# Kernel tuning notes

Hardware: AMD Instinct MI355X
Metric: run time of the kernel (lower is better)

Reference implementation:

```python
import jax, jax.numpy as jnp
import numpy as np

N = 50000      # input_dim == output_dim
E = 800000     # nnz in sparse weight (original: 12300 from w_ind.mat)
B = 64         # batch


def setup_inputs() -> dict:
    key = jax.random.key(0)
    k1, k2, k3, k4, k5 = jax.random.split(key, 5)
    inputs = jax.random.normal(k1, (B, N), dtype=jnp.float32)
    # truncated-normal(std=0.01) approximated by scaled normal
    W3 = 0.01 * jax.random.normal(k2, (E,), dtype=jnp.float32)
    b = jnp.zeros((N,), dtype=jnp.float32)
    # velocity = 1250 * row of CSV -> positive scale vector
    velocity = 1250.0 * jax.random.uniform(k3, (N,), dtype=jnp.float32)
    I = jax.random.randint(k4, (E,), 0, N, dtype=jnp.int64)  # row (dest) index
    J = jax.random.randint(k5, (E,), 0, N, dtype=jnp.int64)  # col (source) index
    return {"inputs": inputs, "W3": W3, "b": b, "velocity": velocity, "I": I, "J": J}


def reference(inputs, W3, b, velocity, I, J):
    # sparse W[i,j] = W3[e] scaled by velocity broadcast along rows -> * velocity[J]
    wv = W3 * velocity[J]                       # [E]
    # out = (W_sparse @ inputs^T)^T + b  == scatter-add over rows I
    contrib = inputs[:, J] * wv[None, :]        # [B, E] gather + scale
    out = jnp.zeros((inputs.shape[0], velocity.shape[0]), inputs.dtype)
    out = out.at[:, I].add(contrib)             # [B, N] scatter-add
    return out + b
```

## Files before the change

### kernel.cpp

```cpp
#include <hip/hip_runtime.h>


#define BATCH 64
#define QROWS 64
#define PCHUNK 8192
#define GCH 512
#define CAP 512

typedef unsigned long long ull;

__global__ void k_prep(const float* __restrict__ in, float* __restrict__ in_T,
                       int* __restrict__ coarse_hist, int NC, int N) {
    const int gid = blockIdx.x * 256 + threadIdx.x;
    if (gid < NC) coarse_hist[gid] = 0;

    __shared__ float tile[64 * 65];
    const int n0 = blockIdx.x * 64;
    const int t  = threadIdx.x;
    const int x  = t & 63;
    const int r  = t >> 6;
    for (int b = r; b < BATCH; b += 4) {
        float v = 0.f;
        if (n0 + x < N) v = in[(size_t)b * N + n0 + x];
        tile[x * 65 + b] = v;
    }
    __syncthreads();
    for (int xr = r; xr < 64; xr += 4) {
        if (n0 + xr < N) in_T[(size_t)(n0 + xr) * BATCH + x] = tile[xr * 65 + x];
    }
}

__global__ void __launch_bounds__(1024) k_hist(const int* __restrict__ I,
                                               int* __restrict__ coarse_hist,
                                               int E, int NC) {
    __shared__ int h[1024];
    const int t = threadIdx.x;
    for (int c = t; c < NC; c += 1024) h[c] = 0;
    __syncthreads();
    const int e0 = blockIdx.x * PCHUNK;
    int e1 = e0 + PCHUNK; if (e1 > E) e1 = E;
    for (int e = e0 + t; e < e1; e += 1024) atomicAdd(&h[I[e] >> 6], 1);
    __syncthreads();
    for (int c = t; c < NC; c += 1024) if (h[c]) atomicAdd(&coarse_hist[c], h[c]);
}

__global__ void __launch_bounds__(1024) k_scan(const int* __restrict__ coarse_hist,
                                               int* __restrict__ coarse_base,
                                               int* __restrict__ gcursor, int NC) {
    __shared__ int sh[1024];
    const int t = threadIdx.x;
    const int v = (t < NC) ? coarse_hist[t] : 0;
    sh[t] = v;
    __syncthreads();
    for (int off = 1; off < 1024; off <<= 1) {
        const int u = (t >= off) ? sh[t - off] : 0;
        __syncthreads();
        sh[t] += u;
        __syncthreads();
    }
    if (t < NC) { coarse_base[t] = sh[t] - v; gcursor[t] = sh[t] - v; }
    if (t == NC - 1) coarse_base[NC] = sh[t];
}

__global__ void __launch_bounds__(1024) k_partition(
        const int* __restrict__ I, const int* __restrict__ J,
        const float* __restrict__ W3, const float* __restrict__ velocity,
        int* __restrict__ gcursor, ull* __restrict__ part, int E, int NC) {
    __shared__ int hist[1024];
    __shared__ int base[1024];
    const int t = threadIdx.x;
    for (int c = t; c < NC; c += 1024) hist[c] = 0;
    __syncthreads();
    const int e0 = blockIdx.x * PCHUNK;
    int e1 = e0 + PCHUNK; if (e1 > E) e1 = E;

    for (int e = e0 + t; e < e1; e += 1024) atomicAdd(&hist[I[e] >> 6], 1);
    __syncthreads();
    for (int c = t; c < NC; c += 1024) {
        const int cnt = hist[c];
        base[c] = cnt ? atomicAdd(&gcursor[c], cnt) : 0;
        hist[c] = 0;
    }
    __syncthreads();
    for (int e = e0 + t; e < e1; e += 1024) {
        const int   i = I[e];
        const int   j = J[e];
        const float w = W3[e] * velocity[j];
        const int   c = i >> 6;
        const int   r = atomicAdd(&hist[c], 1);
        part[(size_t)base[c] + r] = ((ull)__float_as_uint(w) << 32)
                                  | ((ull)((unsigned)(i & 63) << 16) | (unsigned)j);
    }
}

__global__ void __launch_bounds__(512) k_gather(
        const float* __restrict__ in_T, const ull* __restrict__ part,
        const int* __restrict__ coarse_base, const float* __restrict__ bias,
        float* __restrict__ out, int N) {
    __shared__ float tile[64 * 65];
    __shared__ ull   bins[8][CAP];
    __shared__ int   cnt[8];
    const int t    = threadIdx.x;
    const int lane = t & 63;
    const int w    = t >> 6;
    const int c    = blockIdx.x;

    for (int idx = t; idx < 64 * 65; idx += 512) tile[idx] = 0.f;

    const int beg = coarse_base[c];
    const int end = coarse_base[c + 1];

    for (int cb = beg; cb < end; cb += GCH) {
        if (t < 8) cnt[t] = 0;
        __syncthreads();

        const int e = cb + t;
        if (e < end) {
            const ull rec = part[e];
            const int bin = (int)(((unsigned)rec >> 19) & 7u);
            const int r = atomicAdd(&cnt[bin], 1);
            bins[bin][r] = rec;
        }
        __syncthreads();

        const int cw = cnt[w];
        for (int base = 0; base < cw; base += 64) {
            int cc = cw - base; if (cc > 64) cc = 64;
            ull rec = 0ull;
            if (lane < cc) rec = bins[w][base + lane];
            const int rlo = (int)(unsigned)(rec & 0xffffffffu);
            const int rhi = (int)(unsigned)(rec >> 32);
            for (int k0 = 0; k0 < cc; k0 += 8) {
                float v[8], wv[8]; int li[8];
                #pragma unroll
                for (int u = 0; u < 8; ++u) {
                    const int k = k0 + u;
                    const unsigned ij = (unsigned)__shfl(rlo, k);
                    wv[u] = __uint_as_float((unsigned)__shfl(rhi, k));
                    li[u] = (int)((ij >> 16) & 7u);
                    const int j = (int)(ij & 0xffffu);
                    v[u] = in_T[j * BATCH + lane];
                }
                #pragma unroll
                for (int u = 0; u < 8; ++u) {
                    tile[(w * 8 + li[u]) * 65 + lane] += v[u] * wv[u];
                }
            }
        }
        __syncthreads();
    }
    __syncthreads();

    const int n0  = c * QROWS;
    const int row = t & 63;
    const int bq  = t >> 6;
    const int n = n0 + row;
    if (n < N) {
        const float bv = bias[n];
        for (int b = bq; b < BATCH; b += 8)
            out[(size_t)b * N + n] = tile[row * 65 + b] + bv;
    }
}

__global__ void k_edge_scatter_direct(const float* __restrict__ in,
                                      const float* __restrict__ W3,
                                      const float* __restrict__ velocity,
                                      const int* __restrict__ I,
                                      const int* __restrict__ J,
                                      float* __restrict__ out, int N, int E) {
    const int lane = threadIdx.x & 63;
    const long wave   = (long)blockIdx.x * (blockDim.x >> 6) + (threadIdx.x >> 6);
    const long nwaves = (long)gridDim.x * (blockDim.x >> 6);
    for (long base = wave * 64; base < E; base += nwaves * 64) {
        const long e = base + lane;
        int iv = 0, jv = 0; float wvv = 0.f;
        if (e < E) { iv = I[e]; jv = J[e]; wvv = W3[e] * velocity[jv]; }
        const int cnt = (int)((E - base) < 64 ? (E - base) : 64);
        for (int k = 0; k < cnt; ++k) {
            const int   ii = __shfl(iv, k);
            const int   jj = __shfl(jv, k);
            const float wvx = __shfl(wvv, k);
            const float val = in[(size_t)lane * N + jj] * wvx;
            atomicAdd(&out[(size_t)lane * N + ii], val);
        }
    }
}

__global__ void k_add_bias(const float* __restrict__ bias, float* __restrict__ out, int N, int total) {
    int idx = blockIdx.x * blockDim.x + threadIdx.x;
    if (idx < total) out[idx] += bias[idx % N];
}

extern "C" void kernel_launch(void* const* d_in, const int* in_sizes, int n_in,
                              void* d_out, int out_size, void* d_ws, size_t ws_size,
                              hipStream_t stream) {
    const float* inputs   = (const float*)d_in[0];
    const float* W3       = (const float*)d_in[1];
    const float* bias     = (const float*)d_in[2];
    const float* velocity = (const float*)d_in[3];
    const int*   I        = (const int*)d_in[4];
    const int*   J        = (const int*)d_in[5];
    const int E = in_sizes[1];
    const int N = in_sizes[3];
    float* out = (float*)d_out;

    const size_t mat_elems = (size_t)N * BATCH;
    const int NC   = (N + QROWS - 1) / QROWS;
    const int nb_n = (N + 63) / 64;
    const int nb_e = (E + PCHUNK - 1) / PCHUNK;

    const size_t need = mat_elems * sizeof(float)
                      + (size_t)E * sizeof(ull)
                      + (size_t)(NC + (NC + 1) + NC) * sizeof(int);

    if (ws_size >= need && N <= 65535 && NC <= 1024) {
        float* in_T        = (float*)d_ws;
        ull*   part        = (ull*)(in_T + mat_elems);
        int*   coarse_hist = (int*)(part + E);
        int*   coarse_base = coarse_hist + NC;
        int*   gcursor     = coarse_base + NC + 1;

        k_prep     <<<nb_n, 256,  0, stream>>>(inputs, in_T, coarse_hist, NC, N);
        k_hist     <<<nb_e, 1024, 0, stream>>>(I, coarse_hist, E, NC);
        k_scan     <<<1,    1024, 0, stream>>>(coarse_hist, coarse_base, gcursor, NC);
        k_partition<<<nb_e, 1024, 0, stream>>>(I, J, W3, velocity, gcursor, part, E, NC);
        k_gather   <<<NC,   512,  0, stream>>>(in_T, part, coarse_base, bias, out, N);
    } else {
        hipMemsetAsync(out, 0, (size_t)out_size * sizeof(float), stream);
        const int waves_needed   = (E + 63) / 64;
        const int scatter_blocks = (waves_needed + 3) / 4;
        k_edge_scatter_direct<<<scatter_blocks, 256, 0, stream>>>(inputs, W3, velocity, I, J, out, N, E);
        k_add_bias<<<(out_size + 255) / 256, 256, 0, stream>>>(bias, out, N, out_size);
    }
}
```

Before: 161.8 us.

## Bin gather edges per output row and accumulate in registers; single-pass partition

The gather kernel now bins each chunk's edges by their exact destination row (64 bins, capped at 32 entries each, with an overflow list). Each wave accumulates its 8 rows in registers instead of doing read-modify-write on a shared-memory tile. The partition kernel now reads each edge once into registers, ranking it while counting, rather than making two passes over the chunk. Chunk and block sizes shrink to 2048 edges and 512 threads, which gives more blocks. The overflow path is scanned serially by every wave, which could be costly for skewed rows.

Result: faster. 148.9 us (-8.0%).

```diff
diff --git a/kernel.cpp b/kernel.cpp
--- a/kernel.cpp
+++ b/kernel.cpp
@@ -3,9 +3,10 @@
 
 #define BATCH 64
 #define QROWS 64
-#define PCHUNK 8192
+#define PCHUNK 2048
 #define GCH 512
-#define CAP 512
+#define BCAP 32
+#define BSTR 33
 
 typedef unsigned long long ull;
 
@@ -30,18 +31,18 @@
     }
 }
 
-__global__ void __launch_bounds__(1024) k_hist(const int* __restrict__ I,
-                                               int* __restrict__ coarse_hist,
-                                               int E, int NC) {
+__global__ void __launch_bounds__(512) k_hist(const int* __restrict__ I,
+                                              int* __restrict__ coarse_hist,
+                                              int E, int NC) {
     __shared__ int h[1024];
     const int t = threadIdx.x;
-    for (int c = t; c < NC; c += 1024) h[c] = 0;
+    for (int c = t; c < NC; c += 512) h[c] = 0;
     __syncthreads();
     const int e0 = blockIdx.x * PCHUNK;
     int e1 = e0 + PCHUNK; if (e1 > E) e1 = E;
-    for (int e = e0 + t; e < e1; e += 1024) atomicAdd(&h[I[e] >> 6], 1);
-    __syncthreads();
-    for (int c = t; c < NC; c += 1024) if (h[c]) atomicAdd(&coarse_hist[c], h[c]);
+    for (int e = e0 + t; e < e1; e += 512) atomicAdd(&h[I[e] >> 6], 1);
+    __syncthreads();
+    for (int c = t; c < NC; c += 512) if (h[c]) atomicAdd(&coarse_hist[c], h[c]);
 }
 
 __global__ void __launch_bounds__(1024) k_scan(const int* __restrict__ coarse_hist,
@@ -62,93 +63,134 @@
     if (t == NC - 1) coarse_base[NC] = sh[t];
 }
 
-__global__ void __launch_bounds__(1024) k_partition(
+__global__ void __launch_bounds__(512) k_partition(
         const int* __restrict__ I, const int* __restrict__ J,
         const float* __restrict__ W3, const float* __restrict__ velocity,
         int* __restrict__ gcursor, ull* __restrict__ part, int E, int NC) {
     __shared__ int hist[1024];
     __shared__ int base[1024];
     const int t = threadIdx.x;
-    for (int c = t; c < NC; c += 1024) hist[c] = 0;
+    for (int c = t; c < NC; c += 512) hist[c] = 0;
     __syncthreads();
     const int e0 = blockIdx.x * PCHUNK;
     int e1 = e0 + PCHUNK; if (e1 > E) e1 = E;
 
-    for (int e = e0 + t; e < e1; e += 1024) atomicAdd(&hist[I[e] >> 6], 1);
-    __syncthreads();
-    for (int c = t; c < NC; c += 1024) {
+    ull  rec[4];
+    int  cb[4];
+    int  rk[4];
+    bool ok[4];
+    #pragma unroll
+    for (int u = 0; u < 4; ++u) {
+        const int e = e0 + u * 512 + t;
+        ok[u] = (e < e1);
+        cb[u] = 0; rk[u] = 0; rec[u] = 0ull;
+        if (ok[u]) {
+            const int   i = I[e];
+            const int   j = J[e];
+            const float w = W3[e] * velocity[j];
+            cb[u] = i >> 6;
+            rk[u] = atomicAdd(&hist[cb[u]], 1);
+            rec[u] = ((ull)__float_as_uint(w) << 32)
+                   | ((ull)((unsigned)(i & 63) << 16) | (unsigned)j);
+        }
+    }
+    __syncthreads();
+    for (int c = t; c < NC; c += 512) {
         const int cnt = hist[c];
         base[c] = cnt ? atomicAdd(&gcursor[c], cnt) : 0;
-        hist[c] = 0;
-    }
-    __syncthreads();
-    for (int e = e0 + t; e < e1; e += 1024) {
-        const int   i = I[e];
-        const int   j = J[e];
-        const float w = W3[e] * velocity[j];
-        const int   c = i >> 6;
-        const int   r = atomicAdd(&hist[c], 1);
-        part[(size_t)base[c] + r] = ((ull)__float_as_uint(w) << 32)
-                                  | ((ull)((unsigned)(i & 63) << 16) | (unsigned)j);
-    }
+    }
+    __syncthreads();
+    #pragma unroll
+    for (int u = 0; u < 4; ++u)
+        if (ok[u]) part[(size_t)base[cb[u]] + rk[u]] = rec[u];
 }
 
 __global__ void __launch_bounds__(512) k_gather(
         const float* __restrict__ in_T, const ull* __restrict__ part,
         const int* __restrict__ coarse_base, const float* __restrict__ bias,
         float* __restrict__ out, int N) {
-    __shared__ float tile[64 * 65];
-    __shared__ ull   bins[8][CAP];
-    __shared__ int   cnt[8];
+    __shared__ ull smem[64 * BSTR + GCH];
+    __shared__ int cnt[64];
+    __shared__ int ocnt;
+    ull* const bins = smem;
+    ull* const ovf  = smem + 64 * BSTR;
+    float* const tile = (float*)smem;
+
     const int t    = threadIdx.x;
     const int lane = t & 63;
     const int w    = t >> 6;
     const int c    = blockIdx.x;
 
-    for (int idx = t; idx < 64 * 65; idx += 512) tile[idx] = 0.f;
-
     const int beg = coarse_base[c];
     const int end = coarse_base[c + 1];
 
+    float acc[8];
+    #pragma unroll
+    for (int r = 0; r < 8; ++r) acc[r] = 0.f;
+
     for (int cb = beg; cb < end; cb += GCH) {
-        if (t < 8) cnt[t] = 0;
+        __syncthreads();
+        if (t < 64) cnt[t] = 0;
+        if (t == 0) ocnt = 0;
         __syncthreads();
 
         const int e = cb + t;
         if (e < end) {
             const ull rec = part[e];
-            const int bin = (int)(((unsigned)rec >> 19) & 7u);
-            const int r = atomicAdd(&cnt[bin], 1);
-            bins[bin][r] = rec;
-        }
-        __syncthreads();
-
-        const int cw = cnt[w];
-        for (int base = 0; base < cw; base += 64) {
-            int cc = cw - base; if (cc > 64) cc = 64;
-            ull rec = 0ull;
-            if (lane < cc) rec = bins[w][base + lane];
-            const int rlo = (int)(unsigned)(rec & 0xffffffffu);
-            const int rhi = (int)(unsigned)(rec >> 32);
-            for (int k0 = 0; k0 < cc; k0 += 8) {
-                float v[8], wv[8]; int li[8];
-                #pragma unroll
-                for (int u = 0; u < 8; ++u) {
-                    const int k = k0 + u;
-                    const unsigned ij = (unsigned)__shfl(rlo, k);
-                    wv[u] = __uint_as_float((unsigned)__shfl(rhi, k));
-                    li[u] = (int)((ij >> 16) & 7u);
-                    const int j = (int)(ij & 0xffffu);
-                    v[u] = in_T[j * BATCH + lane];
+            const int li = (int)(((unsigned)rec >> 16) & 63u);
+            const int r = atomicAdd(&cnt[li], 1);
+            if (r < BCAP) bins[li * BSTR + r] = rec;
+            else          ovf[atomicAdd(&ocnt, 1)] = rec;
+        }
+        __syncthreads();
+
+        #pragma unroll
+        for (int r8 = 0; r8 < 8; ++r8) {
+            const int row = w * 8 + r8;
+            int n = cnt[row]; if (n > BCAP) n = BCAP;
+            const ull* bp = &bins[row * BSTR];
+            float a = acc[r8];
+            int k = 0;
+            for (; k + 4 <= n; k += 4) {
+                const ull r0 = bp[k], r1 = bp[k + 1], r2 = bp[k + 2], r3 = bp[k + 3];
+                const float v0 = in_T[(int)((unsigned)r0 & 0xffffu) * BATCH + lane];
+                const float v1 = in_T[(int)((unsigned)r1 & 0xffffu) * BATCH + lane];
+                const float v2 = in_T[(int)((unsigned)r2 & 0xffffu) * BATCH + lane];
+                const float v3 = in_T[(int)((unsigned)r3 & 0xffffu) * BATCH + lane];
+                a += v0 * __uint_as_float((unsigned)(r0 >> 32));
+                a += v1 * __uint_as_float((unsigned)(r1 >> 32));
+                a += v2 * __uint_as_float((unsigned)(r2 >> 32));
+                a += v3 * __uint_as_float((unsigned)(r3 >> 32));
+            }
+            for (; k < n; ++k) {
+                const ull rr = bp[k];
+                a += in_T[(int)((unsigned)rr & 0xffffu) * BATCH + lane]
+                   * __uint_as_float((unsigned)(rr >> 32));
+            }
+            acc[r8] = a;
+        }
+
+        const int oc = ocnt;
+        if (oc > 0) {
+            #pragma unroll
+            for (int r8 = 0; r8 < 8; ++r8) {
+                const int row = w * 8 + r8;
+                float a = acc[r8];
+                for (int k = 0; k < oc; ++k) {
+                    const ull rr = ovf[k];
+                    if ((int)(((unsigned)rr >> 16) & 63u) == row)
+                        a += in_T[(int)((unsigned)rr & 0xffffu) * BATCH + lane]
+                           * __uint_as_float((unsigned)(rr >> 32));
                 }
-                #pragma unroll
-                for (int u = 0; u < 8; ++u) {
-                    tile[(w * 8 + li[u]) * 65 + lane] += v[u] * wv[u];
-                }
+                acc[r8] = a;
             }
         }
-        __syncthreads();
-    }
+    }
+
+    __syncthreads();
+    #pragma unroll
+    for (int r8 = 0; r8 < 8; ++r8)
+        tile[(w * 8 + r8) * 65 + lane] = acc[r8];
     __syncthreads();
 
     const int n0  = c * QROWS;
@@ -221,9 +263,9 @@
         int*   gcursor     = coarse_base + NC + 1;
 
         k_prep     <<<nb_n, 256,  0, stream>>>(inputs, in_T, coarse_hist, NC, N);
-        k_hist     <<<nb_e, 1024, 0, stream>>>(I, coarse_hist, E, NC);
+        k_hist     <<<nb_e, 512,  0, stream>>>(I, coarse_hist, E, NC);
         k_scan     <<<1,    1024, 0, stream>>>(coarse_hist, coarse_base, gcursor, NC);
-        k_partition<<<nb_e, 1024, 0, stream>>>(I, J, W3, velocity, gcursor, part, E, NC);
+        k_partition<<<nb_e, 512,  0, stream>>>(I, J, W3, velocity, gcursor, part, E, NC);
         k_gather   <<<NC,   512,  0, stream>>>(in_T, part, coarse_base, bias, out, N);
     } else {
         hipMemsetAsync(out, 0, (size_t)out_size * sizeof(float), stream);
```
